# Kernel tuning notes

Measured on AMD Instinct MI355X. Metric: run time of the kernel, lower is better.

The kernel has to match this reference:

```python
import jax, jax.numpy as jnp
import numpy as np

B, N, C, H = 2, 2048, 1024, 16
D = C // H  # head_dim = 64
EPS = 1e-6


def _rope_freqs(n, d):
    inv_freq = 1.0 / (10000.0 ** (np.arange(0, d // 2, dtype=np.float32) * 2.0 / d))
    ang = np.arange(n, dtype=np.float32)[:, None] * inv_freq[None, :]  # [N, D/2]
    ang = np.concatenate([ang, ang], axis=-1)  # [N, D] (chunk-in-half convention)
    cos = jnp.asarray(np.cos(ang))[None, None]  # [1,1,N,D]
    sin = jnp.asarray(np.sin(ang))[None, None]
    return cos, sin


def setup_inputs() -> dict:
    key = jax.random.key(0)
    k1, k2, k3 = jax.random.split(key, 3)
    x = jax.random.normal(k1, (B, N, C), dtype=jnp.float32)
    w_qkv = jax.random.normal(k2, (3 * C, C), dtype=jnp.float32) * (C ** -0.5)
    w_proj = jax.random.normal(k3, (C, C), dtype=jnp.float32) * (C ** -0.5)
    b_proj = jnp.zeros((C,), dtype=jnp.float32)
    freqs_cos, freqs_sin = _rope_freqs(N, D)
    return {"x": x, "w_qkv": w_qkv, "w_proj": w_proj, "b_proj": b_proj,
            "freqs_cos": freqs_cos, "freqs_sin": freqs_sin}


def _layernorm(t):
    # affine-free LayerNorm over the last (head_dim) axis
    mu = jnp.mean(t, axis=-1, keepdims=True)
    var = jnp.var(t, axis=-1, keepdims=True)
    return (t - mu) * jax.lax.rsqrt(var + EPS)


def _rotate_half(t):
    t1, t2 = jnp.split(t, 2, axis=-1)
    return jnp.concatenate([-t2, t1], axis=-1)


def reference(x, w_qkv, w_proj, b_proj, freqs_cos, freqs_sin):
    b, n, c = x.shape
    qkv = jnp.einsum('bnc,kc->bnk', x, w_qkv)  # [B,N,3C]
    qkv = qkv.reshape(b, n, 3, H, D).transpose(2, 0, 3, 1, 4)  # [3,B,H,N,D]
    q, k, v = qkv[0], qkv[1], qkv[2]
    q = _layernorm(q)
    k = _layernorm(k)
    q = q * freqs_cos + _rotate_half(q) * freqs_sin
    k = k * freqs_cos + _rotate_half(k) * freqs_sin
    scale = D ** -0.5
    scores = jnp.einsum('bhqd,bhkd->bhqk', q, k) * scale  # [B,H,N,N]
    attn = jax.nn.softmax(scores, axis=-1)
    out = jnp.einsum('bhqk,bhkd->bhqd', attn, v)  # [B,H,N,D]
    out = out.transpose(0, 2, 1, 3).reshape(b, n, c)
    return jnp.einsum('bnc,oc->bno', out, w_proj) + b_proj
```

## Files before the change

kernel.cpp:

```cpp
#include <hip/hip_runtime.h>
#include <hip/hip_bf16.h>


typedef __bf16 bf16x8 __attribute__((ext_vector_type(8)));
typedef float f32x4 __attribute__((ext_vector_type(4)));
typedef float f32x16 __attribute__((ext_vector_type(16)));
typedef unsigned short us8 __attribute__((ext_vector_type(8)));
typedef unsigned short us4 __attribute__((ext_vector_type(4)));

static __device__ __forceinline__ unsigned short f2b(float f) {
  __hip_bfloat16 h = __float2bfloat16(f);
  return __builtin_bit_cast(unsigned short, h);
}
static __device__ __forceinline__ float b2f(unsigned short u) {
  __hip_bfloat16 h = __builtin_bit_cast(__hip_bfloat16, u);
  return __bfloat162float(h);
}

#if __has_builtin(__builtin_amdgcn_exp2f)
static __device__ __forceinline__ float fast_exp2(float x) { return __builtin_amdgcn_exp2f(x); }
#else
static __device__ __forceinline__ float fast_exp2(float x) { return exp2f(x); }
#endif

static __device__ __forceinline__ void async_copy16(void* lds, const void* g) {
  __builtin_amdgcn_global_load_lds(
      (const __attribute__((address_space(1))) void*)g,
      (__attribute__((address_space(3))) void*)lds, 16, 0, 0);
}

static __device__ __forceinline__ unsigned cvt_pk_bf16(float lo, float hi) {
  unsigned r;
  asm("v_cvt_pk_bf16_f32 %0, %1, %2" : "=v"(r) : "v"(lo), "v"(hi));
  return r;
}
static __device__ __forceinline__ void swap32(unsigned& x, unsigned& y) {
  asm("v_permlane32_swap_b32 %0, %1" : "+v"(x), "+v"(y));
}
static __device__ __forceinline__ float max3f(float a, float b, float c) {
  float d;
  asm("v_max3_f32 %0, %1, %2, %3" : "=v"(d) : "v"(a), "v"(b), "v"(c));
  return d;
}
static __device__ __forceinline__ float vmax16(const f32x16& v) {
  float a = max3f(v[0], v[1], v[2]);
  float b = max3f(v[3], v[4], v[5]);
  float c = max3f(v[6], v[7], v[8]);
  float d = max3f(v[9], v[10], v[11]);
  float e = max3f(v[12], v[13], v[14]);
  float x = max3f(a, b, c);
  float y = max3f(d, e, v[15]);
  return fmaxf(x, y);
}

__global__ __launch_bounds__(256) void cvt_bf16(
    const float* __restrict__ in, unsigned short* __restrict__ out, int n8) {
  int i = blockIdx.x * 256 + threadIdx.x;
  if (i >= n8) return;
  const float4* p = reinterpret_cast<const float4*>(in) + (size_t)i * 2;
  float4 a = p[0], b = p[1];
  us8 v;
  v[0] = f2b(a.x); v[1] = f2b(a.y); v[2] = f2b(a.z); v[3] = f2b(a.w);
  v[4] = f2b(b.x); v[5] = f2b(b.y); v[6] = f2b(b.z); v[7] = f2b(b.w);
  reinterpret_cast<us8*>(out)[i] = v;
}

__global__ __launch_bounds__(256, 2) void gemm_qkv(
    const unsigned short* __restrict__ A,
    const unsigned short* __restrict__ Bw,
    const float* __restrict__ fcos, const float* __restrict__ fsin,
    unsigned short* __restrict__ qo, unsigned short* __restrict__ ko,
    unsigned short* __restrict__ vt)
{
  __shared__ unsigned short a_sh[128 * 64];
  __shared__ unsigned short b_sh[128 * 64];
  const int tid = threadIdx.x;
  const int lane = tid & 63;
  const int w = tid >> 6;
  const int wr = w >> 1, wc = w & 1;
  const int l15 = lane & 15, l4 = lane >> 4;
  const int m0 = blockIdx.y * 128;
  const int n0 = blockIdx.x * 128;
  const int r8 = lane >> 3, c8 = lane & 7;
  const int K = 1024;

  f32x4 acc[4][4] = {};

  for (int k0 = 0; k0 < K; k0 += 64) {
#pragma unroll
    for (int p = 0; p < 8; ++p) {
      int s = p * 4 + w;
      if (s < 16) {
        int row = s * 8 + r8;
        async_copy16(&a_sh[s * 512],
                     &A[(size_t)(m0 + row) * K + k0 + ((c8 ^ (row & 7)) << 3)]);
      } else {
        int s2 = s - 16;
        int row = s2 * 8 + r8;
        async_copy16(&b_sh[s2 * 512],
                     &Bw[(size_t)(n0 + row) * K + k0 + ((c8 ^ (row & 7)) << 3)]);
      }
    }
    __syncthreads();
#pragma unroll
    for (int kk = 0; kk < 2; ++kk) {
      bf16x8 af[4], bfr[4];
#pragma unroll
      for (int mf = 0; mf < 4; ++mf) {
        int r = wr * 64 + mf * 16 + l15;
        af[mf] = *reinterpret_cast<const bf16x8*>(
            &a_sh[r * 64 + (((kk * 4 + l4) ^ (r & 7)) << 3)]);
      }
#pragma unroll
      for (int nf = 0; nf < 4; ++nf) {
        int r = wc * 64 + nf * 16 + l15;
        bfr[nf] = *reinterpret_cast<const bf16x8*>(
            &b_sh[r * 64 + (((kk * 4 + l4) ^ (r & 7)) << 3)]);
      }
#pragma unroll
      for (int mf = 0; mf < 4; ++mf)
#pragma unroll
        for (int nf = 0; nf < 4; ++nf)
          acc[mf][nf] = __builtin_amdgcn_mfma_f32_16x16x32_bf16(af[mf], bfr[nf], acc[mf][nf], 0, 0, 0);
    }
    __syncthreads();
  }

  const int colbase = n0 + wc * 64;
  const int three = colbase >> 10;
  const int hh = (colbase >> 6) & 15;
  const int b_ = m0 >> 11;
  const int nbase = (m0 & 2047) + wr * 64;
  unsigned short* ep = ((w < 2) ? a_sh : b_sh) + (w & 1) * 4096;
  const int cch = lane & 7, rb2 = lane >> 3;

  if (three < 2) {
    const float sc = three ? 1.f : 0.18033688011112042f;
#pragma unroll
    for (int mf = 0; mf < 4; ++mf) {
#pragma unroll
      for (int j = 0; j < 4; ++j) {
        float a0 = acc[mf][0][j], a1 = acc[mf][1][j];
        float a2 = acc[mf][2][j], a3 = acc[mf][3][j];
        float s1 = (a0 + a1) + (a2 + a3);
        float s2 = (a0 * a0 + a1 * a1) + (a2 * a2 + a3 * a3);
#pragma unroll
        for (int off = 8; off; off >>= 1) {
          s1 += __shfl_xor(s1, off);
          s2 += __shfl_xor(s2, off);
        }
        float mu = s1 * (1.f / 64.f);
        float inv = rsqrtf(s2 * (1.f / 64.f) - mu * mu + 1e-6f);
        int rloc = mf * 16 + l4 * 4 + j;
        int n = nbase + rloc;
        const float* cp = &fcos[(size_t)n * 64];
        const float* sp = &fsin[(size_t)n * 64];
#pragma unroll
        for (int nf = 0; nf < 4; ++nf) {
          int d = nf * 16 + l15;
          float t = (acc[mf][nf][j] - mu) * inv;
          float tp = (acc[mf][nf ^ 2][j] - mu) * inv;
          float r = sc * (t * cp[d] + ((nf < 2) ? -tp : tp) * sp[d]);
          ep[rloc * 64 + ((((d >> 3) ^ (rloc & 7)) << 3) | (d & 7))] = f2b(r);
        }
      }
    }
    unsigned short* dst =
        (three ? ko : qo) + (size_t)(b_ * 16 + hh) * 2048 * 64;
#pragma unroll
    for (int i = 0; i < 8; ++i) {
      int row = i * 8 + rb2;
      us8 vd = *reinterpret_cast<const us8*>(
          &ep[row * 64 + ((cch ^ (row & 7)) << 3)]);
      *reinterpret_cast<us8*>(&dst[(size_t)(nbase + row) * 64 + cch * 8]) = vd;
    }
  } else {
#pragma unroll
    for (int mf = 0; mf < 4; ++mf)
#pragma unroll
      for (int nf = 0; nf < 4; ++nf) {
        int d = nf * 16 + l15;
#pragma unroll
        for (int j = 0; j < 4; ++j) {
          int nl = mf * 16 + l4 * 4 + j;
          ep[d * 64 + ((((nl >> 3) ^ (d & 7)) << 3) | (nl & 7))] =
              f2b(acc[mf][nf][j]);
        }
      }
    unsigned short* dst = vt + (size_t)(b_ * 16 + hh) * 64 * 2048;
#pragma unroll
    for (int i = 0; i < 8; ++i) {
      int d = i * 8 + rb2;
      us8 vd = *reinterpret_cast<const us8*>(
          &ep[d * 64 + ((cch ^ (d & 7)) << 3)]);
      *reinterpret_cast<us8*>(&dst[(size_t)d * 2048 + nbase + cch * 8]) = vd;
    }
  }
}

__global__ __launch_bounds__(256, 2) void gemm_proj(
    const unsigned short* __restrict__ A, const unsigned short* __restrict__ Bw,
    const float* __restrict__ bias, float* __restrict__ Cout,
    int M, int Nn, int K) {
  __shared__ unsigned short a_sh[128 * 64];
  __shared__ unsigned short b_sh[128 * 64];
  const int tid = threadIdx.x;
  const int lane = tid & 63;
  const int w = tid >> 6;
  const int wr = w >> 1, wc = w & 1;
  const int l15 = lane & 15, l4 = lane >> 4;
  const int m0 = blockIdx.y * 128;
  const int n0 = blockIdx.x * 128;
  const int r8 = lane >> 3, c8 = lane & 7;

  f32x4 acc[4][4] = {};

  for (int k0 = 0; k0 < K; k0 += 64) {
#pragma unroll
    for (int p = 0; p < 8; ++p) {
      int s = p * 4 + w;
      if (s < 16) {
        int row = s * 8 + r8;
        async_copy16(&a_sh[s * 512],
                     &A[(size_t)(m0 + row) * K + k0 + ((c8 ^ (row & 7)) << 3)]);
      } else {
        int s2 = s - 16;
        int row = s2 * 8 + r8;
        async_copy16(&b_sh[s2 * 512],
                     &Bw[(size_t)(n0 + row) * K + k0 + ((c8 ^ (row & 7)) << 3)]);
      }
    }
    __syncthreads();
#pragma unroll
    for (int kk = 0; kk < 2; ++kk) {
      bf16x8 af[4], bfr[4];
#pragma unroll
      for (int mf = 0; mf < 4; ++mf) {
        int r = wr * 64 + mf * 16 + l15;
        af[mf] = *reinterpret_cast<const bf16x8*>(
            &a_sh[r * 64 + (((kk * 4 + l4) ^ (r & 7)) << 3)]);
      }
#pragma unroll
      for (int nf = 0; nf < 4; ++nf) {
        int r = wc * 64 + nf * 16 + l15;
        bfr[nf] = *reinterpret_cast<const bf16x8*>(
            &b_sh[r * 64 + (((kk * 4 + l4) ^ (r & 7)) << 3)]);
      }
#pragma unroll
      for (int mf = 0; mf < 4; ++mf)
#pragma unroll
        for (int nf = 0; nf < 4; ++nf)
          acc[mf][nf] = __builtin_amdgcn_mfma_f32_16x16x32_bf16(af[mf], bfr[nf], acc[mf][nf], 0, 0, 0);
    }
    __syncthreads();
  }
#pragma unroll
  for (int mf = 0; mf < 4; ++mf)
#pragma unroll
    for (int nf = 0; nf < 4; ++nf) {
      int col = n0 + wc * 64 + nf * 16 + l15;
#pragma unroll
      for (int j = 0; j < 4; ++j) {
        int row = m0 + wr * 64 + mf * 16 + l4 * 4 + j;
        Cout[(size_t)row * Nn + col] = acc[mf][nf][j] + bias[col];
      }
    }
}

__global__ __launch_bounds__(256, 2) void attn_kern(
    const unsigned short* __restrict__ Q,
    const unsigned short* __restrict__ Kk,
    const unsigned short* __restrict__ Vt,
    unsigned short* __restrict__ O)
{
  __shared__ unsigned short k_sh[2][128 * 64];
  __shared__ unsigned short v_sh[2][64 * 128];
  const int tid = threadIdx.x;
  const int lane = tid & 63;
  const int w = tid >> 6;
  const int l31 = lane & 31;
  const int H = lane >> 5;
  const int bid = blockIdx.x;
  const int wid = (bid & 7) * 64 + (bid >> 3);
  const int qt = wid & 15;
  const int bh = wid >> 4;
  const int h = bh & 15, b = bh >> 4;
  const unsigned short* qb = Q + (size_t)bh * 2048 * 64;
  const unsigned short* kb = Kk + (size_t)bh * 2048 * 64;
  const unsigned short* vb = Vt + (size_t)bh * 64 * 2048;
  const int tok = qt * 128 + w * 32 + l31;

  bf16x8 qf[4];
#pragma unroll
  for (int c = 0; c < 4; ++c)
    qf[c] = *reinterpret_cast<const bf16x8*>(&qb[(size_t)tok * 64 + c * 16 + H * 8]);

  f32x16 oT[2] = {};
  float mr = -1e30f, lr = 0.f;

  const int r8 = lane >> 3, cc8 = lane & 7;
  const int r4 = lane >> 4, cc16 = lane & 15;
#define ATTN_STAGE(KT, BUF)                                                           \
  {                                                                                   \
    _Pragma("unroll") for (int p = 0; p < 8; ++p) {                                   \
      int sseg = p * 4 + w;                                                           \
      if (sseg < 16) {                                                                \
        int row = sseg * 8 + r8;                                                      \
        async_copy16(&k_sh[BUF][sseg * 512],                                          \
                     &kb[(size_t)((KT) * 128 + row) * 64 + ((cc8 ^ (row & 7)) << 3)]);   \
      } else {                                                                        \
        int s2 = sseg - 16;                                                           \
        int row = s2 * 4 + r4;                                                        \
        async_copy16(&v_sh[BUF][s2 * 512],                                            \
                     &vb[(size_t)row * 2048 + (KT) * 128 + ((cc16 ^ (row & 7)) << 3)]);  \
      }                                                                               \
    }                                                                                 \
  }

  ATTN_STAGE(0, 0);
  __syncthreads();

  for (int kt = 0; kt < 16; ++kt) {
    const int cur = kt & 1;
    if (kt < 15) ATTN_STAGE(kt + 1, cur ^ 1);

    f32x16 sT[4] = {};
    __builtin_amdgcn_s_setprio(1);
#pragma unroll
    for (int c = 0; c < 4; ++c) {
      int ch0 = 2 * c + H;
#pragma unroll
      for (int t = 0; t < 4; ++t) {
        int r = t * 32 + l31;
        bf16x8 ka = *reinterpret_cast<const bf16x8*>(
            &k_sh[cur][r * 64 + (((ch0) ^ (r & 7)) << 3)]);
        sT[t] = __builtin_amdgcn_mfma_f32_32x32x16_bf16(ka, qf[c], sT[t], 0, 0, 0);
      }
    }
    __builtin_amdgcn_s_setprio(0);
    float tmax = fmaxf(fmaxf(vmax16(sT[0]), vmax16(sT[1])),
                       fmaxf(vmax16(sT[2]), vmax16(sT[3])));
    tmax = fmaxf(tmax, __shfl_xor(tmax, 32));
    if (__any(tmax > mr + 8.f)) {
      float mn = fmaxf(mr, tmax);
      float corr = fast_exp2(mr - mn);
      mr = mn;
      lr *= corr;
#pragma unroll
      for (int r = 0; r < 16; ++r) { oT[0][r] *= corr; oT[1][r] *= corr; }
    }
    float tsum = 0.f;
#pragma unroll
    for (int t = 0; t < 4; ++t)
#pragma unroll
      for (int r = 0; r < 16; ++r) {
        float p = fast_exp2(sT[t][r] - mr);
        sT[t][r] = p;
        tsum += p;
      }
    tsum += __shfl_xor(tsum, 32);
    lr += tsum;

    bf16x8 pB[8];
#pragma unroll
    for (int t = 0; t < 4; ++t)
#pragma unroll
      for (int half = 0; half < 2; ++half) {
        const int base = 8 * half;
        unsigned x0 = cvt_pk_bf16(sT[t][base + 0], sT[t][base + 1]);
        unsigned x1 = cvt_pk_bf16(sT[t][base + 2], sT[t][base + 3]);
        unsigned y0 = cvt_pk_bf16(sT[t][base + 4], sT[t][base + 5]);
        unsigned y1 = cvt_pk_bf16(sT[t][base + 6], sT[t][base + 7]);
        swap32(x0, y0);
        swap32(x1, y1);
        int4 packed = {(int)x0, (int)x1, (int)y0, (int)y1};
        pB[2 * t + half] = __builtin_bit_cast(bf16x8, packed);
      }
    __builtin_amdgcn_s_setprio(1);
#pragma unroll
    for (int dt = 0; dt < 2; ++dt) {
      int r = dt * 32 + l31;
#pragma unroll
      for (int mi = 0; mi < 8; ++mi) {
        int ch = (mi * 2 + H) ^ (r & 7);
        bf16x8 va = *reinterpret_cast<const bf16x8*>(&v_sh[cur][r * 128 + (ch << 3)]);
        oT[dt] = __builtin_amdgcn_mfma_f32_32x32x16_bf16(va, pB[mi], oT[dt], 0, 0, 0);
      }
    }
    __builtin_amdgcn_s_setprio(0);
    __syncthreads();
  }
  float invl = 1.f / lr;
#pragma unroll
  for (int dt = 0; dt < 2; ++dt)
#pragma unroll
    for (int rb = 0; rb < 4; ++rb) {
      us4 ov;
#pragma unroll
      for (int j = 0; j < 4; ++j) ov[j] = f2b(oT[dt][rb * 4 + j] * invl);
      *reinterpret_cast<us4*>(
          &O[((size_t)b * 2048 + tok) * 1024 + h * 64 + 32 * dt + 8 * rb + 4 * H]) = ov;
    }
#undef ATTN_STAGE
}

extern "C" void kernel_launch(void* const* d_in, const int* in_sizes, int n_in,
                              void* d_out, int out_size, void* d_ws, size_t ws_size,
                              hipStream_t stream) {
  (void)in_sizes; (void)n_in; (void)out_size; (void)ws_size;
  const float* x      = (const float*)d_in[0];
  const float* w_qkv  = (const float*)d_in[1];
  const float* w_proj = (const float*)d_in[2];
  const float* b_proj = (const float*)d_in[3];
  const float* fcos   = (const float*)d_in[4];
  const float* fsin   = (const float*)d_in[5];
  float* out = (float*)d_out;
  char* ws = (char*)d_ws;

  unsigned short* x_bf     = (unsigned short*)(ws + 0);
  unsigned short* wqkv_bf  = (unsigned short*)(ws + 8388608);
  unsigned short* wproj_bf = (unsigned short*)(ws + 14680064);
  unsigned short* q_bf     = (unsigned short*)(ws + 16777216);
  unsigned short* k_bf     = (unsigned short*)(ws + 25165824);
  unsigned short* vt_bf    = (unsigned short*)(ws + 33554432);
  unsigned short* ao_bf    = (unsigned short*)(ws + 41943040);

  cvt_bf16<<<2048, 256, 0, stream>>>(x, x_bf, 4096 * 1024 / 8);
  cvt_bf16<<<1536, 256, 0, stream>>>(w_qkv, wqkv_bf, 3072 * 1024 / 8);
  cvt_bf16<<<512, 256, 0, stream>>>(w_proj, wproj_bf, 1024 * 1024 / 8);
  gemm_qkv<<<dim3(24, 32), 256, 0, stream>>>(x_bf, wqkv_bf, fcos, fsin,
                                             q_bf, k_bf, vt_bf);
  attn_kern<<<512, 256, 0, stream>>>(q_bf, k_bf, vt_bf, ao_bf);
  gemm_proj<<<dim3(8, 32), 256, 0, stream>>>(ao_bf, wproj_bf, b_proj, out,
                                             4096, 1024, 1024);
}
```

Measured before the change: 124.4 us.

## Fuse bf16 conversions, raise qkv GEMM occupancy, drop setprio, defer row-sum shuffle

Merges the three fp32-to-bf16 conversion launches into a single kernel that picks its source by index range, removing two launch overheads. Raises gemm_qkv launch bounds to three blocks per CU, which may constrain registers. In attention, drops the s_setprio wave priority hints and moves the cross-half softmax denominator shuffle out of the kv loop to a single shuffle at the end. The deferred sum stays correct because the rescale factor is uniform across both halves.

```diff
diff --git a/kernel.cpp b/kernel.cpp
--- a/kernel.cpp
+++ b/kernel.cpp
@@ -53,19 +53,30 @@
   return fmaxf(x, y);
 }
 
-__global__ __launch_bounds__(256) void cvt_bf16(
-    const float* __restrict__ in, unsigned short* __restrict__ out, int n8) {
+__global__ __launch_bounds__(256) void cvt_all(
+    const float* __restrict__ x, const float* __restrict__ wqkv,
+    const float* __restrict__ wproj, unsigned short* __restrict__ x_bf,
+    unsigned short* __restrict__ wqkv_bf, unsigned short* __restrict__ wproj_bf) {
   int i = blockIdx.x * 256 + threadIdx.x;
-  if (i >= n8) return;
-  const float4* p = reinterpret_cast<const float4*>(in) + (size_t)i * 2;
+  const float* src;
+  unsigned short* dst;
+  int off;
+  if (i < 524288) {
+    src = x; dst = x_bf; off = i;
+  } else if (i < 917504) {
+    src = wqkv; dst = wqkv_bf; off = i - 524288;
+  } else {
+    src = wproj; dst = wproj_bf; off = i - 917504;
+  }
+  const float4* p = reinterpret_cast<const float4*>(src) + (size_t)off * 2;
   float4 a = p[0], b = p[1];
   us8 v;
   v[0] = f2b(a.x); v[1] = f2b(a.y); v[2] = f2b(a.z); v[3] = f2b(a.w);
   v[4] = f2b(b.x); v[5] = f2b(b.y); v[6] = f2b(b.z); v[7] = f2b(b.w);
-  reinterpret_cast<us8*>(out)[i] = v;
-}
-
-__global__ __launch_bounds__(256, 2) void gemm_qkv(
+  reinterpret_cast<us8*>(dst)[off] = v;
+}
+
+__global__ __launch_bounds__(256, 3) void gemm_qkv(
     const unsigned short* __restrict__ A,
     const unsigned short* __restrict__ Bw,
     const float* __restrict__ fcos, const float* __restrict__ fsin,
@@ -158,9 +169,9 @@
 #pragma unroll
         for (int nf = 0; nf < 4; ++nf) {
           int d = nf * 16 + l15;
-          float t = (acc[mf][nf][j] - mu) * inv;
+          float tt = (acc[mf][nf][j] - mu) * inv;
           float tp = (acc[mf][nf ^ 2][j] - mu) * inv;
-          float r = sc * (t * cp[d] + ((nf < 2) ? -tp : tp) * sp[d]);
+          float r = sc * (tt * cp[d] + ((nf < 2) ? -tp : tp) * sp[d]);
           ep[rloc * 64 + ((((d >> 3) ^ (rloc & 7)) << 3) | (d & 7))] = f2b(r);
         }
       }
@@ -325,7 +336,6 @@
     if (kt < 15) ATTN_STAGE(kt + 1, cur ^ 1);
 
     f32x16 sT[4] = {};
-    __builtin_amdgcn_s_setprio(1);
 #pragma unroll
     for (int c = 0; c < 4; ++c) {
       int ch0 = 2 * c + H;
@@ -337,7 +347,6 @@
         sT[t] = __builtin_amdgcn_mfma_f32_32x32x16_bf16(ka, qf[c], sT[t], 0, 0, 0);
       }
     }
-    __builtin_amdgcn_s_setprio(0);
     float tmax = fmaxf(fmaxf(vmax16(sT[0]), vmax16(sT[1])),
                        fmaxf(vmax16(sT[2]), vmax16(sT[3])));
     tmax = fmaxf(tmax, __shfl_xor(tmax, 32));
@@ -358,7 +367,6 @@
         sT[t][r] = p;
         tsum += p;
       }
-    tsum += __shfl_xor(tsum, 32);
     lr += tsum;
 
     bf16x8 pB[8];
@@ -376,7 +384,6 @@
         int4 packed = {(int)x0, (int)x1, (int)y0, (int)y1};
         pB[2 * t + half] = __builtin_bit_cast(bf16x8, packed);
       }
-    __builtin_amdgcn_s_setprio(1);
 #pragma unroll
     for (int dt = 0; dt < 2; ++dt) {
       int r = dt * 32 + l31;
@@ -387,9 +394,9 @@
         oT[dt] = __builtin_amdgcn_mfma_f32_32x32x16_bf16(va, pB[mi], oT[dt], 0, 0, 0);
       }
     }
-    __builtin_amdgcn_s_setprio(0);
     __syncthreads();
   }
+  lr += __shfl_xor(lr, 32);
   float invl = 1.f / lr;
 #pragma unroll
   for (int dt = 0; dt < 2; ++dt)
@@ -425,9 +432,7 @@
   unsigned short* vt_bf    = (unsigned short*)(ws + 33554432);
   unsigned short* ao_bf    = (unsigned short*)(ws + 41943040);
 
-  cvt_bf16<<<2048, 256, 0, stream>>>(x, x_bf, 4096 * 1024 / 8);
-  cvt_bf16<<<1536, 256, 0, stream>>>(w_qkv, wqkv_bf, 3072 * 1024 / 8);
-  cvt_bf16<<<512, 256, 0, stream>>>(w_proj, wproj_bf, 1024 * 1024 / 8);
+  cvt_all<<<4096, 256, 0, stream>>>(x, w_qkv, w_proj, x_bf, wqkv_bf, wproj_bf);
   gemm_qkv<<<dim3(24, 32), 256, 0, stream>>>(x_bf, wqkv_bf, fcos, fsin,
                                              q_bf, k_bf, vt_bf);
   attn_kern<<<512, 256, 0, stream>>>(q_bf, k_bf, vt_bf, ao_bf);
```

Result: faster. 116.5 us (-6.3%).
